# Kernel optimization log

Measured on AMD Instinct MI355X. Metric: run time of the kernel, lower is better.

## Reference

```python
import jax, jax.numpy as jnp
import numpy as np

N_VOXELS = 200000
DIM = 96
KVOL = 343  # 7^3 depthwise kernel offsets
N_EDGES = 3200000


def setup_inputs() -> dict:
    key = jax.random.key(0)
    ks = jax.random.split(key, 10)
    feats = jax.random.normal(ks[0], (N_VOXELS, DIM), dtype=jnp.float32)
    w_dw = jax.random.normal(ks[1], (KVOL, DIM), dtype=jnp.float32) * 0.02
    b_dw = jax.random.normal(ks[2], (DIM,), dtype=jnp.float32) * 0.02
    ln_w = jnp.ones((DIM,), dtype=jnp.float32)
    ln_b = jnp.zeros((DIM,), dtype=jnp.float32)
    w1 = jax.random.normal(ks[3], (DIM, 4 * DIM), dtype=jnp.float32) * 0.02
    b1 = jax.random.normal(ks[4], (4 * DIM,), dtype=jnp.float32) * 0.02
    w2 = jax.random.normal(ks[5], (4 * DIM, DIM), dtype=jnp.float32) * 0.02
    b2 = jax.random.normal(ks[6], (DIM,), dtype=jnp.float32) * 0.02
    in_idx = jax.random.randint(ks[7], (N_EDGES,), 0, N_VOXELS, dtype=jnp.int32)
    out_idx = jax.random.randint(ks[8], (N_EDGES,), 0, N_VOXELS, dtype=jnp.int32)
    kernel_idx = jax.random.randint(ks[9], (N_EDGES,), 0, KVOL, dtype=jnp.int32)
    return {"feats": feats, "w_dw": w_dw, "b_dw": b_dw, "ln_w": ln_w,
            "ln_b": ln_b, "w1": w1, "b1": b1, "w2": w2, "b2": b2,
            "in_idx": in_idx, "out_idx": out_idx, "kernel_idx": kernel_idx}


def reference(feats, w_dw, b_dw, ln_w, ln_b, w1, b1, w2, b2,
              in_idx, out_idx, kernel_idx):
    n = feats.shape[0]
    # sparse depthwise conv via kernel-map gather/scatter:
    # out[o, c] += feats[i, c] * w_dw[k, c] for each edge (i, o, k)
    contrib = feats[in_idx] * w_dw[kernel_idx]           # [E, C]
    x = jax.ops.segment_sum(contrib, out_idx, num_segments=n) + b_dw
    # LayerNorm over channels, eps=1e-6
    mu = jnp.mean(x, axis=-1, keepdims=True)
    var = jnp.mean(jnp.square(x - mu), axis=-1, keepdims=True)
    x = (x - mu) * jax.lax.rsqrt(var + 1e-6) * ln_w + ln_b
    # pointwise MLP with exact GELU
    h = jax.nn.gelu(x @ w1 + b1, approximate=False)      # [N, 4C]
    x = h @ w2 + b2                                      # [N, C]
    # residual (drop_path rate 0.0 -> identity)
    return feats + x
```

## Files before the change

### kernel.cpp

```cpp
#include <hip/hip_runtime.h>
#include <hip/hip_bf16.h>

#define NVOX 200000
#define DIM 96
#define KVOL 343
#define NEDGE 3200000
#define HID 384
#define TM 32
#define SLOT_CAP 64

typedef __attribute__((ext_vector_type(8))) __bf16 bf16x8;
typedef __attribute__((ext_vector_type(4))) __bf16 bf16x4;
typedef __attribute__((ext_vector_type(4))) float f32x4;
typedef __attribute__((ext_vector_type(4))) int i32x4;

__global__ void prep(const float* __restrict__ feats, const float* __restrict__ w1,
                     const float* __restrict__ w2, const float* __restrict__ w_dw,
                     __bf16* __restrict__ featsb, __hip_bfloat16* __restrict__ w1t,
                     __hip_bfloat16* __restrict__ w2t, __bf16* __restrict__ wdwb,
                     int* __restrict__ cnt) {
    int t = blockIdx.x * 256 + threadIdx.x;
    f32x4 v = __builtin_nontemporal_load((const f32x4*)(feats + t * 4));
    bf16x4 o;
    o[0] = (__bf16)v.x; o[1] = (__bf16)v.y; o[2] = (__bf16)v.z; o[3] = (__bf16)v.w;
    __builtin_nontemporal_store(o, (bf16x4*)(featsb + t * 4));
    if (t < HID * DIM) {
        int n1 = t / DIM, k1 = t % DIM;
        w1t[t] = __float2bfloat16(w1[k1 * HID + n1]);
        int n2 = t / HID, k2 = t % HID;
        w2t[t] = __float2bfloat16(w2[k2 * DIM + n2]);
        if (t < KVOL * DIM) wdwb[t] = (__bf16)w_dw[t];
    }
    if (t < NVOX) cnt[t] = 0;
}

__global__ void scatter_T(const i32x4* __restrict__ in4, const i32x4* __restrict__ out4,
                          const i32x4* __restrict__ k4, int* __restrict__ cnt,
                          unsigned* __restrict__ slots) {
    int t = blockIdx.x * 256 + threadIdx.x;
    i32x4 i = __builtin_nontemporal_load(&in4[t]);
    i32x4 o = __builtin_nontemporal_load(&out4[t]);
    i32x4 k = __builtin_nontemporal_load(&k4[t]);
    int d;
    d = atomicAdd(&cnt[o.x], 1);
    if (d < SLOT_CAP) slots[d * NVOX + o.x] = (unsigned)i.x | ((unsigned)k.x << 18);
    d = atomicAdd(&cnt[o.y], 1);
    if (d < SLOT_CAP) slots[d * NVOX + o.y] = (unsigned)i.y | ((unsigned)k.y << 18);
    d = atomicAdd(&cnt[o.z], 1);
    if (d < SLOT_CAP) slots[d * NVOX + o.z] = (unsigned)i.z | ((unsigned)k.z << 18);
    d = atomicAdd(&cnt[o.w], 1);
    if (d < SLOT_CAP) slots[d * NVOX + o.w] = (unsigned)i.w | ((unsigned)k.w << 18);
}

__global__ __launch_bounds__(256, 4) void fused_all(
    const __bf16* __restrict__ featsb, const __bf16* __restrict__ wdwb,
    const float* __restrict__ b_dw,
    const float* __restrict__ ln_w, const float* __restrict__ ln_b,
    const __hip_bfloat16* __restrict__ w1t, const float* __restrict__ b1,
    const __hip_bfloat16* __restrict__ w2t, const float* __restrict__ b2,
    const unsigned* __restrict__ slots, const int* __restrict__ cnt,
    float* __restrict__ out)
{
    __shared__ __hip_bfloat16 At[TM][104];
    __shared__ __align__(16) char shb[TM * 200 * 2];
    __hip_bfloat16 (*Ht)[200] = (__hip_bfloat16 (*)[200])shb;
    unsigned (*recsL)[68] = (unsigned (*)[68])shb;

    const int t   = threadIdx.x;
    const int blk = blockIdx.x;

    {
        const int row  = t >> 3;
        const int sub  = t & 7;
        const int part = sub & 3;
        const int half = sub >> 2;
        const int c0   = part * 24;
        const int v    = blk * TM + row;

        int c = cnt[v];
        if (c > SLOT_CAP) c = SLOT_CAP;

        for (int d = sub; d < c; d += 8)
            recsL[row][d] = slots[d * NVOX + v];
        __syncthreads();

        float xa[24];
        #pragma unroll
        for (int j = 0; j < 24; ++j) xa[j] = 0.f;

        const __bf16* fbase = featsb + c0;
        const __bf16* wbase = wdwb + c0;
        const unsigned* rl = recsL[row];

        const int e_lo = half ? (c >> 1) : 0;
        const int e_hi = half ? c : (c >> 1);

#define LDE(F, W, ee) { unsigned rr = rl[ee]; \
        const __bf16* fr = fbase + (int)(rr & 0x3FFFFu) * DIM; \
        const __bf16* wr = wbase + (int)(rr >> 18) * DIM; \
        F##0 = *(const bf16x8*)(fr);      W##0 = *(const bf16x8*)(wr); \
        F##1 = *(const bf16x8*)(fr + 8);  W##1 = *(const bf16x8*)(wr + 8); \
        F##2 = *(const bf16x8*)(fr + 16); W##2 = *(const bf16x8*)(wr + 16); }

#define ACC(F, W) { \
        _Pragma("unroll") for (int j = 0; j < 8; ++j) xa[j]      += (float)F##0[j] * (float)W##0[j]; \
        _Pragma("unroll") for (int j = 0; j < 8; ++j) xa[8 + j]  += (float)F##1[j] * (float)W##1[j]; \
        _Pragma("unroll") for (int j = 0; j < 8; ++j) xa[16 + j] += (float)F##2[j] * (float)W##2[j]; }

        bf16x8 Af0, Af1, Af2, Aw0, Aw1, Aw2, Bf0, Bf1, Bf2, Bw0, Bw1, Bw2;
        int e = e_lo;
        if (e + 2 <= e_hi) {
            LDE(Af, Aw, e); LDE(Bf, Bw, e + 1);
            e += 2;
            for (; e + 2 <= e_hi; e += 2) {
                bf16x8 Cf0, Cf1, Cf2, Cw0, Cw1, Cw2, Df0, Df1, Df2, Dw0, Dw1, Dw2;
                LDE(Cf, Cw, e); LDE(Df, Dw, e + 1);
                ACC(Af, Aw); ACC(Bf, Bw);
                Af0 = Cf0; Af1 = Cf1; Af2 = Cf2; Aw0 = Cw0; Aw1 = Cw1; Aw2 = Cw2;
                Bf0 = Df0; Bf1 = Df1; Bf2 = Df2; Bw0 = Dw0; Bw1 = Dw1; Bw2 = Dw2;
            }
            ACC(Af, Aw); ACC(Bf, Bw);
        }
        if (e < e_hi) {
            LDE(Af, Aw, e);
            ACC(Af, Aw);
        }
#undef LDE
#undef ACC

        #pragma unroll
        for (int j = 0; j < 24; ++j) xa[j] += __shfl_xor(xa[j], 4);

        float s = 0.f, s2 = 0.f;
        #pragma unroll
        for (int j = 0; j < 24; ++j) {
            float x = xa[j] + b_dw[c0 + j];
            xa[j] = x;
            s += x; s2 += x * x;
        }
        s  += __shfl_xor(s, 1);  s  += __shfl_xor(s, 2);
        s2 += __shfl_xor(s2, 1); s2 += __shfl_xor(s2, 2);
        float mean = s * (1.f / 96.f);
        float var  = s2 * (1.f / 96.f) - mean * mean;
        float rstd = rsqrtf(var + 1e-6f);

        if (half == 0) {
            #pragma unroll
            for (int jj = 0; jj < 3; ++jj) {
                bf16x8 pack;
                #pragma unroll
                for (int j = 0; j < 8; ++j) {
                    int cch = c0 + jj*8 + j;
                    float xn = (xa[jj*8+j] - mean) * rstd * ln_w[cch] + ln_b[cch];
                    pack[j] = (__bf16)xn;
                }
                *(bf16x8*)&At[row][c0 + jj*8] = pack;
            }
        }
    }
    __syncthreads();

    const int w  = t >> 6;
    const int l  = t & 63;
    const int lr = l & 15;
    const int lk = l >> 4;
    const int rb = w >> 1;
    const int jh = w & 1;

    f32x4 acc2[3];
    #pragma unroll
    for (int j = 0; j < 3; ++j) acc2[j] = (f32x4){0.f, 0.f, 0.f, 0.f};

    #pragma unroll
    for (int h = 0; h < 2; ++h) {
        f32x4 acc[6];
        #pragma unroll
        for (int j = 0; j < 6; ++j) acc[j] = (f32x4){0.f, 0.f, 0.f, 0.f};

        #pragma unroll
        for (int kk = 0; kk < 3; ++kk) {
            bf16x8 a = *(const bf16x8*)&At[rb*16 + lr][kk*32 + lk*8];
            #pragma unroll
            for (int j = 0; j < 6; ++j) {
                int col = h*192 + jh*96 + j*16 + lr;
                bf16x8 b = *(const bf16x8*)&w1t[col * DIM + kk*32 + lk*8];
                acc[j] = __builtin_amdgcn_mfma_f32_16x16x32_bf16(a, b, acc[j], 0, 0, 0);
            }
        }

        if (h == 1) __syncthreads();

        #pragma unroll
        for (int j = 0; j < 6; ++j) {
            int col = h*192 + jh*96 + j*16 + lr;
            float bb = b1[col];
            #pragma unroll
            for (int r = 0; r < 4; ++r) {
                float vv = acc[j][r] + bb;
                float ge = 0.5f * vv * (1.f + erff(vv * 0.70710678f));
                Ht[rb*16 + lk*4 + r][jh*96 + j*16 + lr] = __float2bfloat16(ge);
            }
        }
        __syncthreads();

        #pragma unroll
        for (int kk = 0; kk < 6; ++kk) {
            bf16x8 a = *(const bf16x8*)&Ht[rb*16 + lr][kk*32 + lk*8];
            #pragma unroll
            for (int j = 0; j < 3; ++j) {
                int col = jh*48 + j*16 + lr;
                bf16x8 b = *(const bf16x8*)&w2t[col * HID + (h*6 + kk)*32 + lk*8];
                acc2[j] = __builtin_amdgcn_mfma_f32_16x16x32_bf16(a, b, acc2[j], 0, 0, 0);
            }
        }
    }

    #pragma unroll
    for (int j = 0; j < 3; ++j) {
        int col = jh*48 + j*16 + lr;
        float bb = b2[col];
        #pragma unroll
        for (int r = 0; r < 4; ++r) {
            int grow = blk * TM + rb*16 + lk*4 + r;
            int off = grow * DIM + col;
            float res = (float)featsb[off];
            __builtin_nontemporal_store(acc2[j][r] + bb + res, &out[off]);
        }
    }
}

extern "C" void kernel_launch(void* const* d_in, const int* in_sizes, int n_in,
                              void* d_out, int out_size, void* d_ws, size_t ws_size,
                              hipStream_t stream) {
    const float* feats = (const float*)d_in[0];
    const float* w_dw  = (const float*)d_in[1];
    const float* b_dw  = (const float*)d_in[2];
    const float* ln_w  = (const float*)d_in[3];
    const float* ln_b  = (const float*)d_in[4];
    const float* w1    = (const float*)d_in[5];
    const float* b1    = (const float*)d_in[6];
    const float* w2    = (const float*)d_in[7];
    const float* b2    = (const float*)d_in[8];
    const int* in_idx  = (const int*)d_in[9];
    const int* out_idx = (const int*)d_in[10];
    const int* k_idx   = (const int*)d_in[11];
    float* out = (float*)d_out;

    char* ws = (char*)d_ws;
    unsigned* slots = (unsigned*)ws;
    int* cnt   = (int*)(ws + 51200000);
    __hip_bfloat16* w1t = (__hip_bfloat16*)(ws + 52000000);
    __hip_bfloat16* w2t = (__hip_bfloat16*)(ws + 52073728);
    __bf16* wdwb = (__bf16*)(ws + 52147456);
    __bf16* featsb = (__bf16*)(ws + 52213312);

    prep<<<(NVOX * DIM / 4) / 256, 256, 0, stream>>>(feats, w1, w2, w_dw,
                                                     featsb, w1t, w2t, wdwb, cnt);
    scatter_T<<<NEDGE / 4 / 256, 256, 0, stream>>>((const i32x4*)in_idx,
                                                   (const i32x4*)out_idx,
                                                   (const i32x4*)k_idx, cnt, slots);
    fused_all<<<NVOX / TM, 256, 0, stream>>>(featsb, wdwb, b_dw, ln_w, ln_b,
                                             w1t, b1, w2t, b2, slots, cnt, out);
}
```

Before: 477.7 us.

## Merge prep and scatter kernels, interleave gather channel layout, raise occupancy

Zeroing of the counters moves into its own small kernel, and the bf16 conversion is merged with the edge scatter into one launch so the two independent workloads run concurrently across CUs. The gather channel assignment changes from contiguous 24-channel chunks to interleaved 8-channel groups at strides of 32, so the four lanes of a row read adjacent 16-byte segments together and coalesce better. The launch bounds minimum blocks per CU goes from 4 to 6, which may force register spills in the fused kernel.

```diff
diff --git a/kernel.cpp b/kernel.cpp
--- a/kernel.cpp
+++ b/kernel.cpp
@@ -8,51 +8,57 @@
 #define HID 384
 #define TM 32
 #define SLOT_CAP 64
+#define NPREP (NVOX * DIM / 4 / 256)
+#define NSCAT (NEDGE / 4 / 256)
 
 typedef __attribute__((ext_vector_type(8))) __bf16 bf16x8;
 typedef __attribute__((ext_vector_type(4))) __bf16 bf16x4;
 typedef __attribute__((ext_vector_type(4))) float f32x4;
 typedef __attribute__((ext_vector_type(4))) int i32x4;
 
-__global__ void prep(const float* __restrict__ feats, const float* __restrict__ w1,
-                     const float* __restrict__ w2, const float* __restrict__ w_dw,
-                     __bf16* __restrict__ featsb, __hip_bfloat16* __restrict__ w1t,
-                     __hip_bfloat16* __restrict__ w2t, __bf16* __restrict__ wdwb,
-                     int* __restrict__ cnt) {
-    int t = blockIdx.x * 256 + threadIdx.x;
-    f32x4 v = __builtin_nontemporal_load((const f32x4*)(feats + t * 4));
-    bf16x4 o;
-    o[0] = (__bf16)v.x; o[1] = (__bf16)v.y; o[2] = (__bf16)v.z; o[3] = (__bf16)v.w;
-    __builtin_nontemporal_store(o, (bf16x4*)(featsb + t * 4));
-    if (t < HID * DIM) {
-        int n1 = t / DIM, k1 = t % DIM;
-        w1t[t] = __float2bfloat16(w1[k1 * HID + n1]);
-        int n2 = t / HID, k2 = t % HID;
-        w2t[t] = __float2bfloat16(w2[k2 * DIM + n2]);
-        if (t < KVOL * DIM) wdwb[t] = (__bf16)w_dw[t];
-    }
-    if (t < NVOX) cnt[t] = 0;
-}
-
-__global__ void scatter_T(const i32x4* __restrict__ in4, const i32x4* __restrict__ out4,
-                          const i32x4* __restrict__ k4, int* __restrict__ cnt,
-                          unsigned* __restrict__ slots) {
-    int t = blockIdx.x * 256 + threadIdx.x;
-    i32x4 i = __builtin_nontemporal_load(&in4[t]);
-    i32x4 o = __builtin_nontemporal_load(&out4[t]);
-    i32x4 k = __builtin_nontemporal_load(&k4[t]);
-    int d;
-    d = atomicAdd(&cnt[o.x], 1);
-    if (d < SLOT_CAP) slots[d * NVOX + o.x] = (unsigned)i.x | ((unsigned)k.x << 18);
-    d = atomicAdd(&cnt[o.y], 1);
-    if (d < SLOT_CAP) slots[d * NVOX + o.y] = (unsigned)i.y | ((unsigned)k.y << 18);
-    d = atomicAdd(&cnt[o.z], 1);
-    if (d < SLOT_CAP) slots[d * NVOX + o.z] = (unsigned)i.z | ((unsigned)k.z << 18);
-    d = atomicAdd(&cnt[o.w], 1);
-    if (d < SLOT_CAP) slots[d * NVOX + o.w] = (unsigned)i.w | ((unsigned)k.w << 18);
-}
-
-__global__ __launch_bounds__(256, 4) void fused_all(
+__global__ void zero_cnt(int* __restrict__ cnt) {
+    int i = blockIdx.x * 256 + threadIdx.x;
+    if (i < NVOX) cnt[i] = 0;
+}
+
+__global__ void prep_scatter(const float* __restrict__ feats, const float* __restrict__ w1,
+                             const float* __restrict__ w2, const float* __restrict__ w_dw,
+                             __bf16* __restrict__ featsb, __hip_bfloat16* __restrict__ w1t,
+                             __hip_bfloat16* __restrict__ w2t, __bf16* __restrict__ wdwb,
+                             const i32x4* __restrict__ in4, const i32x4* __restrict__ out4,
+                             const i32x4* __restrict__ k4, int* __restrict__ cnt,
+                             unsigned* __restrict__ slots) {
+    if (blockIdx.x < NPREP) {
+        int t = blockIdx.x * 256 + threadIdx.x;
+        f32x4 v = __builtin_nontemporal_load((const f32x4*)(feats + t * 4));
+        bf16x4 o;
+        o[0] = (__bf16)v.x; o[1] = (__bf16)v.y; o[2] = (__bf16)v.z; o[3] = (__bf16)v.w;
+        __builtin_nontemporal_store(o, (bf16x4*)(featsb + t * 4));
+        if (t < HID * DIM) {
+            int n1 = t / DIM, k1 = t % DIM;
+            w1t[t] = __float2bfloat16(w1[k1 * HID + n1]);
+            int n2 = t / HID, k2 = t % HID;
+            w2t[t] = __float2bfloat16(w2[k2 * DIM + n2]);
+            if (t < KVOL * DIM) wdwb[t] = (__bf16)w_dw[t];
+        }
+    } else {
+        int t = (blockIdx.x - NPREP) * 256 + threadIdx.x;
+        i32x4 i = __builtin_nontemporal_load(&in4[t]);
+        i32x4 o = __builtin_nontemporal_load(&out4[t]);
+        i32x4 k = __builtin_nontemporal_load(&k4[t]);
+        int d;
+        d = atomicAdd(&cnt[o.x], 1);
+        if (d < SLOT_CAP) slots[d * NVOX + o.x] = (unsigned)i.x | ((unsigned)k.x << 18);
+        d = atomicAdd(&cnt[o.y], 1);
+        if (d < SLOT_CAP) slots[d * NVOX + o.y] = (unsigned)i.y | ((unsigned)k.y << 18);
+        d = atomicAdd(&cnt[o.z], 1);
+        if (d < SLOT_CAP) slots[d * NVOX + o.z] = (unsigned)i.z | ((unsigned)k.z << 18);
+        d = atomicAdd(&cnt[o.w], 1);
+        if (d < SLOT_CAP) slots[d * NVOX + o.w] = (unsigned)i.w | ((unsigned)k.w << 18);
+    }
+}
+
+__global__ __launch_bounds__(256, 6) void fused_all(
     const __bf16* __restrict__ featsb, const __bf16* __restrict__ wdwb,
     const float* __restrict__ b_dw,
     const float* __restrict__ ln_w, const float* __restrict__ ln_b,
@@ -74,7 +80,7 @@
         const int sub  = t & 7;
         const int part = sub & 3;
         const int half = sub >> 2;
-        const int c0   = part * 24;
+        const int cb   = part * 8;
         const int v    = blk * TM + row;
 
         int c = cnt[v];
@@ -88,8 +94,8 @@
         #pragma unroll
         for (int j = 0; j < 24; ++j) xa[j] = 0.f;
 
-        const __bf16* fbase = featsb + c0;
-        const __bf16* wbase = wdwb + c0;
+        const __bf16* fbase = featsb + cb;
+        const __bf16* wbase = wdwb + cb;
         const unsigned* rl = recsL[row];
 
         const int e_lo = half ? (c >> 1) : 0;
@@ -99,8 +105,8 @@
         const __bf16* fr = fbase + (int)(rr & 0x3FFFFu) * DIM; \
         const __bf16* wr = wbase + (int)(rr >> 18) * DIM; \
         F##0 = *(const bf16x8*)(fr);      W##0 = *(const bf16x8*)(wr); \
-        F##1 = *(const bf16x8*)(fr + 8);  W##1 = *(const bf16x8*)(wr + 8); \
-        F##2 = *(const bf16x8*)(fr + 16); W##2 = *(const bf16x8*)(wr + 16); }
+        F##1 = *(const bf16x8*)(fr + 32); W##1 = *(const bf16x8*)(wr + 32); \
+        F##2 = *(const bf16x8*)(fr + 64); W##2 = *(const bf16x8*)(wr + 64); }
 
 #define ACC(F, W) { \
         _Pragma("unroll") for (int j = 0; j < 8; ++j) xa[j]      += (float)F##0[j] * (float)W##0[j]; \
@@ -133,10 +139,13 @@
 
         float s = 0.f, s2 = 0.f;
         #pragma unroll
-        for (int j = 0; j < 24; ++j) {
-            float x = xa[j] + b_dw[c0 + j];
-            xa[j] = x;
-            s += x; s2 += x * x;
+        for (int jj = 0; jj < 3; ++jj) {
+            #pragma unroll
+            for (int j = 0; j < 8; ++j) {
+                float x = xa[jj*8+j] + b_dw[jj*32 + cb + j];
+                xa[jj*8+j] = x;
+                s += x; s2 += x * x;
+            }
         }
         s  += __shfl_xor(s, 1);  s  += __shfl_xor(s, 2);
         s2 += __shfl_xor(s2, 1); s2 += __shfl_xor(s2, 2);
@@ -150,11 +159,11 @@
                 bf16x8 pack;
                 #pragma unroll
                 for (int j = 0; j < 8; ++j) {
-                    int cch = c0 + jj*8 + j;
+                    int cch = jj*32 + cb + j;
                     float xn = (xa[jj*8+j] - mean) * rstd * ln_w[cch] + ln_b[cch];
                     pack[j] = (__bf16)xn;
                 }
-                *(bf16x8*)&At[row][c0 + jj*8] = pack;
+                *(bf16x8*)&At[row][jj*32 + cb] = pack;
             }
         }
     }
@@ -254,11 +263,10 @@
     __bf16* wdwb = (__bf16*)(ws + 52147456);
     __bf16* featsb = (__bf16*)(ws + 52213312);
 
-    prep<<<(NVOX * DIM / 4) / 256, 256, 0, stream>>>(feats, w1, w2, w_dw,
-                                                     featsb, w1t, w2t, wdwb, cnt);
-    scatter_T<<<NEDGE / 4 / 256, 256, 0, stream>>>((const i32x4*)in_idx,
-                                                   (const i32x4*)out_idx,
-                                                   (const i32x4*)k_idx, cnt, slots);
+    zero_cnt<<<(NVOX + 255) / 256, 256, 0, stream>>>(cnt);
+    prep_scatter<<<NPREP + NSCAT, 256, 0, stream>>>(
+        feats, w1, w2, w_dw, featsb, w1t, w2t, wdwb,
+        (const i32x4*)in_idx, (const i32x4*)out_idx, (const i32x4*)k_idx, cnt, slots);
     fused_all<<<NVOX / TM, 256, 0, stream>>>(featsb, wdwb, b_dw, ln_w, ln_b,
                                              w1t, b1, w2t, b2, slots, cnt, out);
 }
```

After: 898.2 us. +88.0%, slower.
